# Kernel tuning notes

Hardware: AMD Instinct MI355X
Metric: run time of the kernel (lower is better)

## Reference

```python
import jax, jax.numpy as jnp
import numpy as np

DIM, K_RANK, L, N_CLASS = 64, 16, 8, 10
H = 1e-3
B = 256
DD = DIM * DIM  # 4096


def _cay(C, D):
    # Cayley transform of B = C @ D^T : I + C (I - 0.5 D^T C)^{-1} D^T
    Id = jnp.eye(C.shape[1], dtype=C.dtype)
    DT = jnp.swapaxes(D, 1, 2)
    inv = jnp.linalg.inv(Id - 0.5 * DT @ C)
    return Id + C @ inv @ DT


def setup_inputs() -> dict:
    key = jax.random.key(0)
    ks = jax.random.split(key, 9)
    u = jax.random.normal(ks[0], (B, DIM, K_RANK), jnp.float32) / np.float32(np.sqrt(DIM))
    vh = jax.random.normal(ks[1], (B, K_RANK, DIM), jnp.float32) / np.float32(np.sqrt(DIM))
    eye_k = jnp.eye(K_RANK, dtype=jnp.float32)
    off = 0.05 * jax.random.normal(ks[2], (B, K_RANK, K_RANK), jnp.float32) * (1.0 - eye_k)
    dvals = jax.random.uniform(ks[3], (B, K_RANK), jnp.float32, 0.5, 1.5)
    s_core = off + dvals[:, :, None] * eye_k  # diag bounded away from 0 (invert_S)
    s_block = jnp.zeros((B, DIM, K_RANK), jnp.float32).at[:, :K_RANK, :K_RANK].set(s_core)
    X = jnp.stack([u.reshape(B, -1), s_block.reshape(B, -1), vh.reshape(B, -1)], axis=1)
    sc = np.float32(1.0 / np.sqrt(DD))
    W0 = sc * jax.random.normal(ks[4], (DD, DD), jnp.float32)
    W = sc * jax.random.normal(ks[5], (L, DD, DD), jnp.float32)
    b = sc * jax.random.normal(ks[6], (L, DD), jnp.float32)
    Wc = sc * jax.random.normal(ks[7], (N_CLASS, DD), jnp.float32)
    bc = sc * jax.random.normal(ks[8], (N_CLASS,), jnp.float32)
    return {"X": X, "W0": W0, "W": W, "b": b, "Wc": Wc, "bc": bc}


def reference(X, W0, W, b, Wc, bc):
    Bn = X.shape[0]
    u = X[:, 0].reshape(Bn, DIM, K_RANK)
    s = X[:, 1].reshape(Bn, DIM, K_RANK)[:, :K_RANK, :K_RANK]
    vh = X[:, 2].reshape(Bn, K_RANK, DIM)
    v = jnp.swapaxes(vh, 1, 2)
    eye_k = jnp.eye(K_RANK, dtype=X.dtype)
    eye_d = jnp.eye(DIM, dtype=X.dtype)
    Xf = (u @ s @ vh).reshape(Bn, DD)
    outs = []
    for i in range(L + 1):  # layer 0 has no bias
        lin = Xf @ W0.T if i == 0 else Xf @ W[i - 1].T + b[i - 1]
        dY = jax.nn.relu(lin).reshape(Bn, DIM, DIM)
        # invert_S: invert only the diagonal of s
        s_inv = (1.0 / jnp.diagonal(s, axis1=1, axis2=2))[:, :, None] * eye_k
        dU = dY @ v @ s_inv
        dV = jnp.swapaxes(dY, 1, 2) @ u @ jnp.swapaxes(s_inv, 1, 2)
        dS = jnp.swapaxes(u, 1, 2) @ dY @ v
        uT = jnp.swapaxes(u, 1, 2)
        F = (eye_d - u @ uT) @ dU
        FT = jnp.swapaxes(F, 1, 2)
        u = _cay(H * (F @ uT), -H * (u @ FT)) @ u
        vT = jnp.swapaxes(v, 1, 2)
        F = (eye_d - v @ vT) @ dV
        FT = jnp.swapaxes(F, 1, 2)
        v = _cay(H * (F @ vT), -H * (v @ FT)) @ v
        s = s + H * dS
        Xf = (u @ s @ jnp.swapaxes(v, 1, 2)).reshape(Bn, DD)
        outs.append(Xf)
    X_transformed = jnp.stack(outs, axis=-1)  # (B, dim*dim, L+1)
    X_classified = Xf @ Wc.T + bc
    X_predicted = jax.nn.softmax(X_classified, axis=1)
    return X_predicted, X_classified, X_transformed
```

## Files before the change

### kernel.cpp

```cpp
#include <hip/hip_runtime.h>
#include <math.h>

typedef unsigned short u16;
typedef unsigned int u32;
using bf16x8 = __attribute__((ext_vector_type(8))) short;
using f32x4  = __attribute__((ext_vector_type(4))) float;

#define DD 4096
#define NB 256
#define SPLIT_K 4
#define PSTRIDE (NB * DD)
#define PLANE (NB * DD)

__device__ __forceinline__ u16 f2bf(float f) {
  unsigned int u = __float_as_uint(f);
  u += 0x7fffu + ((u >> 16) & 1u);
  return (u16)(u >> 16);
}
__device__ __forceinline__ float bf2f(u16 h) {
  return __uint_as_float((u32)h << 16);
}
__device__ __forceinline__ unsigned int pack2bf(float a, float b) {
  return (unsigned int)f2bf(a) | ((unsigned int)f2bf(b) << 16);
}
__device__ __forceinline__ void async_cp16(const u16* g, u16* l) {
  __builtin_amdgcn_global_load_lds(
      (const __attribute__((address_space(1))) unsigned int*)g,
      (__attribute__((address_space(3))) unsigned int*)l, 16, 0, 0);
}

__global__ __launch_bounds__(512) void gemm_kernel(
    const u16* __restrict__ A, const float* __restrict__ W,
    u16* __restrict__ part)
{
  const int nt = blockIdx.x;
  const int kz = blockIdx.y;
  const int t = threadIdx.x;
  const int w = t >> 6, l = t & 63;

  __shared__ __align__(16) u16 As[3][256 * 64];
  __shared__ __align__(16) u16 Bs[2][64 * 64];

  const int colg0 = nt << 6;
  const int k0 = kz << 10;

  f32x4 acc[4][2];
#pragma unroll
  for (int mi = 0; mi < 4; ++mi)
#pragma unroll
    for (int nj = 0; nj < 2; ++nj)
      acc[mi][nj] = (f32x4){0.f, 0.f, 0.f, 0.f};

  const int wm = w & 3, wn = w >> 2;
  const int lr = l & 15, lg = l >> 4;
  const int arow_l = (w << 3) + (l >> 3);
  const int acl = l & 7;
  const int bn_l = t >> 3;
  const int bcc = t & 7;

  float4 bs0[3], bs1[3];

#define ISSUE_A(tt, buf) do {                                                \
    const int kkk = k0 + ((tt) << 6);                                        \
    _Pragma("unroll")                                                        \
    for (int r = 0; r < 4; ++r) {                                            \
      const int row = (r << 6) + arow_l;                                     \
      const int cs = acl ^ (row & 7);                                        \
      async_cp16(A + ((size_t)row << 12) + kkk + (cs << 3),                  \
                 &As[buf][(r << 12) + (w << 9)]);                            \
    } } while (0)

#define LOAD_B(tt, set) do {                                                 \
    const float* wsrc = W + ((size_t)(colg0 + bn_l) << 12) + k0 +            \
                        ((tt) << 6) + (bcc << 3);                            \
    bs0[set] = *reinterpret_cast<const float4*>(wsrc);                       \
    bs1[set] = *reinterpret_cast<const float4*>(wsrc + 4);                   \
  } while (0)

  ISSUE_A(0, 0); LOAD_B(0, 0);
  ISSUE_A(1, 1); LOAD_B(1, 1);

#pragma unroll
  for (int tt = 0; tt < 16; ++tt) {
    const int cb = tt % 3, nb = (tt + 2) % 3, pb = tt & 1;
    if (tt + 2 < 16) { ISSUE_A(tt + 2, nb); LOAD_B(tt + 2, nb); }
    if (tt < 14)       { asm volatile("s_waitcnt vmcnt(12)" ::: "memory"); }
    else if (tt == 14) { asm volatile("s_waitcnt vmcnt(6)"  ::: "memory"); }
    else               { asm volatile("s_waitcnt vmcnt(0)"  ::: "memory"); }
    __builtin_amdgcn_sched_barrier(0);
    {
      uint4 pk;
      pk.x = pack2bf(bs0[cb].x, bs0[cb].y);
      pk.y = pack2bf(bs0[cb].z, bs0[cb].w);
      pk.z = pack2bf(bs1[cb].x, bs1[cb].y);
      pk.w = pack2bf(bs1[cb].z, bs1[cb].w);
      *reinterpret_cast<uint4*>(&Bs[pb][(bn_l << 6) + ((bcc ^ (bn_l & 7)) << 3)]) = pk;
    }
    asm volatile("s_waitcnt lgkmcnt(0)" ::: "memory");
    __builtin_amdgcn_s_barrier();
    __builtin_amdgcn_sched_barrier(0);
#pragma unroll
    for (int ks = 0; ks < 2; ++ks) {
      const int cg = (ks << 2) + lg;
      bf16x8 av[4], bv[2];
#pragma unroll
      for (int mi = 0; mi < 4; ++mi) {
        const int fr = (wm << 6) + (mi << 4) + lr;
        av[mi] = *reinterpret_cast<const bf16x8*>(&As[cb][(fr << 6) + ((cg ^ (fr & 7)) << 3)]);
      }
#pragma unroll
      for (int nj = 0; nj < 2; ++nj) {
        const int fc = (wn << 5) + (nj << 4) + lr;
        bv[nj] = *reinterpret_cast<const bf16x8*>(&Bs[pb][(fc << 6) + ((cg ^ (fc & 7)) << 3)]);
      }
#pragma unroll
      for (int mi = 0; mi < 4; ++mi)
#pragma unroll
        for (int nj = 0; nj < 2; ++nj)
          acc[mi][nj] = __builtin_amdgcn_mfma_f32_16x16x32_bf16(
              av[mi], bv[nj], acc[mi][nj], 0, 0, 0);
    }
    __builtin_amdgcn_s_barrier();
  }
#undef ISSUE_A
#undef LOAD_B

  u16* pout = part + (size_t)kz * PSTRIDE;
#pragma unroll
  for (int mi = 0; mi < 4; ++mi)
#pragma unroll
    for (int nj = 0; nj < 2; ++nj) {
      const int col = colg0 + (wn << 5) + (nj << 4) + lr;
#pragma unroll
      for (int j = 0; j < 4; ++j) {
        const int row = (wm << 6) + (mi << 4) + (lg << 2) + j;
        pout[((size_t)row << 12) + col] = f2bf(acc[mi][nj][j]);
      }
    }
}

__device__ __forceinline__ void stiefel_update512(
    float (&Am)[64][17], float (&Dm)[64][17], float (&Fm)[64][17],
    float (&T1)[16][17], float (&G1)[16][17], float (&G2)[16][17],
    float (&M1)[16][17], float (&RS)[512],
    int t, float* __restrict__ gout, size_t ub)
{
  const int p = t >> 3;
  const int j0 = (t << 1) & 15;
  {
    const int half = t & 1, i = t >> 5, j = (t >> 1) & 15;
    float a = 0.f;
    const int r0 = half << 5;
    for (int r = r0; r < r0 + 32; ++r) a += Am[r][i] * Dm[r][j];
    RS[t] = a;
  }
  __syncthreads();
  if (t < 256) T1[t >> 4][t & 15] = RS[t << 1] + RS[(t << 1) + 1];
  __syncthreads();
  {
    float f0 = Dm[p][j0], f1 = Dm[p][j0 + 1];
    for (int k = 0; k < 16; ++k) {
      const float ak = Am[p][k];
      f0 -= ak * T1[k][j0];
      f1 -= ak * T1[k][j0 + 1];
    }
    Fm[p][j0] = f0; Fm[p][j0 + 1] = f1;
  }
  __syncthreads();
  if (t < 256) {
    const int i = t >> 4, j = t & 15;
    float g = 0.f;
    for (int r = 0; r < 64; ++r) g += Am[r][i] * Fm[r][j];
    G1[i][j] = g;
  } else {
    const int tt = t - 256, i = tt >> 4, j = tt & 15;
    float g = 0.f;
    for (int r = 0; r < 64; ++r) g += Am[r][i] * Am[r][j];
    G2[i][j] = g;
  }
  __syncthreads();
  if (t < 256) {
    const int i = t >> 4, j = t & 15;
    float m = 0.f;
    for (int k = 0; k < 16; ++k) m += G1[i][k] * G2[k][j];
    M1[i][j] = m;
  }
  __syncthreads();
  {
    float a0 = 0.f, a1 = 0.f;
    for (int k = 0; k < 16; ++k) {
      const float fk = Fm[p][k];
      a0 += fk * M1[k][j0];
      a1 += fk * M1[k][j0 + 1];
    }
    const float n0 = Am[p][j0] - 1e-6f * a0;
    const float n1 = Am[p][j0 + 1] - 1e-6f * a1;
    __syncthreads();
    Am[p][j0] = n0; Am[p][j0 + 1] = n1;
    *reinterpret_cast<float2*>(gout + ub + (p << 4) + j0) = make_float2(n0, n1);
  }
  __syncthreads();
}

__global__ __launch_bounds__(512) void update_kernel(
    const u16* __restrict__ part, const float* __restrict__ bias,
    float* __restrict__ u_g, float* __restrict__ v_g, float* __restrict__ s_g,
    float* __restrict__ Xf, u16* __restrict__ Xfb,
    float* __restrict__ outL, int layer)
{
  const int b = blockIdx.x, t = threadIdx.x;
  __shared__ float dY[64][68];
  __shared__ float U[64][17], V[64][17];
  __shared__ float P[64][17], Q[64][17], F[64][17];
  __shared__ float S[16][16], dSs[16][17], T1[16][17], G1[16][17], G2[16][17], M1[16][17];
  __shared__ float sinv[16];
  __shared__ float RS[512];

  const size_t ub = (size_t)b << 10;
  {
    const float2 u2 = *reinterpret_cast<const float2*>(u_g + ub + (t << 1));
    const float2 v2 = *reinterpret_cast<const float2*>(v_g + ub + (t << 1));
    const int r = t >> 3, c = (t & 7) << 1;
    U[r][c] = u2.x; U[r][c + 1] = u2.y;
    V[r][c] = v2.x; V[r][c + 1] = v2.y;
    if (t < 256) S[t >> 4][t & 15] = s_g[((size_t)b << 8) + t];
  }
  __syncthreads();
  if (t < 16) sinv[t] = 1.0f / S[t][t];
  {
    const u16* p0 = part + ((size_t)b << 12) + (t << 3);
    float x[8];
#pragma unroll
    for (int e = 0; e < 8; ++e) x[e] = 0.f;
#pragma unroll
    for (int kzi = 0; kzi < 4; ++kzi) {
      const uint4 v = *reinterpret_cast<const uint4*>(p0 + (size_t)kzi * PSTRIDE);
      x[0] += bf2f((u16)(v.x & 0xffff)); x[1] += bf2f((u16)(v.x >> 16));
      x[2] += bf2f((u16)(v.y & 0xffff)); x[3] += bf2f((u16)(v.y >> 16));
      x[4] += bf2f((u16)(v.z & 0xffff)); x[5] += bf2f((u16)(v.z >> 16));
      x[6] += bf2f((u16)(v.w & 0xffff)); x[7] += bf2f((u16)(v.w >> 16));
    }
    if (bias != nullptr) {
      const float4 b0 = *reinterpret_cast<const float4*>(bias + (t << 3));
      const float4 b1 = *reinterpret_cast<const float4*>(bias + (t << 3) + 4);
      x[0] += b0.x; x[1] += b0.y; x[2] += b0.z; x[3] += b0.w;
      x[4] += b1.x; x[5] += b1.y; x[6] += b1.z; x[7] += b1.w;
    }
    const int r = t >> 3, c = (t & 7) << 3;
    float4* d0 = reinterpret_cast<float4*>(&dY[r][c]);
    d0[0] = make_float4(fmaxf(x[0], 0.f), fmaxf(x[1], 0.f), fmaxf(x[2], 0.f), fmaxf(x[3], 0.f));
    d0[1] = make_float4(fmaxf(x[4], 0.f), fmaxf(x[5], 0.f), fmaxf(x[6], 0.f), fmaxf(x[7], 0.f));
  }
  __syncthreads();
  const int p = t >> 3;
  const int j0 = (t << 1) & 15;
  {
    float a0 = 0.f, a1 = 0.f;
    for (int q = 0; q < 64; ++q) {
      const float d = dY[p][q];
      a0 += d * V[q][j0];
      a1 += d * V[q][j0 + 1];
    }
    P[p][j0] = a0; P[p][j0 + 1] = a1;
    float b0 = 0.f, b1 = 0.f;
    for (int r = 0; r < 64; ++r) {
      const float d = dY[r][p];
      b0 += d * U[r][j0];
      b1 += d * U[r][j0 + 1];
    }
    Q[p][j0] = b0; Q[p][j0 + 1] = b1;
  }
  __syncthreads();
  {
    const int half = t & 1, i = t >> 5, j = (t >> 1) & 15;
    float a = 0.f;
    const int r0 = half << 5;
    for (int r = r0; r < r0 + 32; ++r) a += U[r][i] * P[r][j];
    RS[t] = a;
  }
  __syncthreads();
  if (t < 256) dSs[t >> 4][t & 15] = RS[t << 1] + RS[(t << 1) + 1];
  __syncthreads();
  for (int i = t; i < 1024; i += 512) {
    const int r = i >> 4, c = i & 15;
    const float sc = sinv[c];
    P[r][c] *= sc;
    Q[r][c] *= sc;
  }
  __syncthreads();

  stiefel_update512(U, P, F, T1, G1, G2, M1, RS, t, u_g, ub);
  stiefel_update512(V, Q, F, T1, G1, G2, M1, RS, t, v_g, ub);

  if (t < 256) {
    const int i = t >> 4, j = t & 15;
    const float ns = S[i][j] + 1e-3f * dSs[i][j];
    S[i][j] = ns;
    s_g[((size_t)b << 8) + t] = ns;
  }
  __syncthreads();
  {
    float a0 = 0.f, a1 = 0.f;
    for (int k = 0; k < 16; ++k) {
      const float uk = U[p][k];
      a0 += uk * S[k][j0];
      a1 += uk * S[k][j0 + 1];
    }
    P[p][j0] = a0; P[p][j0 + 1] = a1;
  }
  __syncthreads();
  {
    const int q0 = (t & 7) << 3;
    float res[8];
#pragma unroll
    for (int e = 0; e < 8; ++e) res[e] = 0.f;
    for (int i = 0; i < 16; ++i) {
      const float pi = P[p][i];
#pragma unroll
      for (int e = 0; e < 8; ++e) res[e] += pi * V[q0 + e][i];
    }
    const size_t ko = ((size_t)b << 12) + (p << 6) + q0;
    float4* xo = reinterpret_cast<float4*>(Xf + ko);
    xo[0] = make_float4(res[0], res[1], res[2], res[3]);
    xo[1] = make_float4(res[4], res[5], res[6], res[7]);
    uint4 pk;
    pk.x = pack2bf(res[0], res[1]); pk.y = pack2bf(res[2], res[3]);
    pk.z = pack2bf(res[4], res[5]); pk.w = pack2bf(res[6], res[7]);
    *reinterpret_cast<uint4*>(Xfb + ko) = pk;
    float4* op = reinterpret_cast<float4*>(outL + (size_t)layer * PLANE + ko);
    op[0] = xo[0]; op[1] = xo[1];
  }
}

__global__ __launch_bounds__(256) void pack_kernel(
    const float* __restrict__ outL, float* __restrict__ outT)
{
  const int t = threadIdx.x;
  const int base = blockIdx.x << 8;
  __shared__ float buf[256 * 9];
#pragma unroll
  for (int l = 0; l < 9; ++l)
    buf[t * 9 + l] = outL[(size_t)l * PLANE + base + t];
  __syncthreads();
  const float4* b4 = reinterpret_cast<const float4*>(buf);
  float4* o4 = reinterpret_cast<float4*>(outT + (size_t)base * 9);
  for (int i = t; i < 576; i += 256) o4[i] = b4[i];
}

__global__ __launch_bounds__(256) void init_kernel(
    const float* __restrict__ X, float* __restrict__ u_g, float* __restrict__ v_g,
    float* __restrict__ s_g, float* __restrict__ Xf, u16* __restrict__ Xfb)
{
  const int b = blockIdx.x, t = threadIdx.x;
  __shared__ float U[64][17], V[64][17], S[16][16], P[64][17];
  const float* xb = X + (size_t)b * 3072;
  const size_t ub = (size_t)b << 10;
  {
    const float4 u4 = *reinterpret_cast<const float4*>(xb + (t << 2));
    const int r = t >> 2, c = (t & 3) << 2;
    U[r][c] = u4.x; U[r][c + 1] = u4.y; U[r][c + 2] = u4.z; U[r][c + 3] = u4.w;
    *reinterpret_cast<float4*>(u_g + ub + (t << 2)) = u4;
    const float sv = xb[1024 + t];
    S[t >> 4][t & 15] = sv;
    s_g[((size_t)b << 8) + t] = sv;
    const float4 v4 = *reinterpret_cast<const float4*>(xb + 2048 + (t << 2));
    const int g = t << 2;
    const int iv = g >> 6, q = g & 63;
    V[q][iv] = v4.x; V[q + 1][iv] = v4.y; V[q + 2][iv] = v4.z; V[q + 3][iv] = v4.w;
    v_g[ub + (size_t)q * 16 + iv] = v4.x;
    v_g[ub + (size_t)(q + 1) * 16 + iv] = v4.y;
    v_g[ub + (size_t)(q + 2) * 16 + iv] = v4.z;
    v_g[ub + (size_t)(q + 3) * 16 + iv] = v4.w;
  }
  __syncthreads();
  const int p4 = t >> 2, e4 = (t & 3) << 2;
#pragma unroll
  for (int e = 0; e < 4; ++e) {
    float a = 0.f;
    for (int i = 0; i < 16; ++i) a += U[p4][i] * S[i][e4 + e];
    P[p4][e4 + e] = a;
  }
  __syncthreads();
  {
    const int q0 = (t & 3) << 4;
    float res[16];
#pragma unroll
    for (int qq = 0; qq < 16; ++qq) {
      float a = 0.f;
      for (int i = 0; i < 16; ++i) a += P[p4][i] * V[q0 + qq][i];
      res[qq] = a;
    }
    const size_t ko = ((size_t)b << 12) + (p4 << 6) + q0;
    float4* xo = reinterpret_cast<float4*>(Xf + ko);
    xo[0] = make_float4(res[0], res[1], res[2], res[3]);
    xo[1] = make_float4(res[4], res[5], res[6], res[7]);
    xo[2] = make_float4(res[8], res[9], res[10], res[11]);
    xo[3] = make_float4(res[12], res[13], res[14], res[15]);
    uint4 pk0, pk1;
    pk0.x = pack2bf(res[0], res[1]);   pk0.y = pack2bf(res[2], res[3]);
    pk0.z = pack2bf(res[4], res[5]);   pk0.w = pack2bf(res[6], res[7]);
    pk1.x = pack2bf(res[8], res[9]);   pk1.y = pack2bf(res[10], res[11]);
    pk1.z = pack2bf(res[12], res[13]); pk1.w = pack2bf(res[14], res[15]);
    *reinterpret_cast<uint4*>(Xfb + ko) = pk0;
    *reinterpret_cast<uint4*>(Xfb + ko + 8) = pk1;
  }
}

__global__ __launch_bounds__(256) void classifier_kernel(
    const float* __restrict__ Xf, const float* __restrict__ Wc,
    const float* __restrict__ bc, float* __restrict__ pred, float* __restrict__ cls)
{
  const int b = blockIdx.x, t = threadIdx.x;
  const int lane = t & 63, w = t >> 6;
  __shared__ float red[4][10];
  float acc[10];
#pragma unroll
  for (int c = 0; c < 10; ++c) acc[c] = 0.f;
  const float* xr = Xf + ((size_t)b << 12);
  for (int k = t; k < 4096; k += 256) {
    const float x = xr[k];
#pragma unroll
    for (int c = 0; c < 10; ++c) acc[c] += x * Wc[c * 4096 + k];
  }
#pragma unroll
  for (int c = 0; c < 10; ++c)
    for (int off = 32; off; off >>= 1) acc[c] += __shfl_xor(acc[c], off);
  if (lane == 0)
#pragma unroll
    for (int c = 0; c < 10; ++c) red[w][c] = acc[c];
  __syncthreads();
  if (t == 0) {
    float lg[10], ex[10];
    float m = -1e30f;
#pragma unroll
    for (int c = 0; c < 10; ++c) {
      lg[c] = red[0][c] + red[1][c] + red[2][c] + red[3][c] + bc[c];
      m = fmaxf(m, lg[c]);
    }
    float s = 0.f;
#pragma unroll
    for (int c = 0; c < 10; ++c) { ex[c] = expf(lg[c] - m); s += ex[c]; }
    const float inv = 1.f / s;
#pragma unroll
    for (int c = 0; c < 10; ++c) {
      cls[b * 10 + c] = lg[c];
      pred[b * 10 + c] = ex[c] * inv;
    }
  }
}

extern "C" void kernel_launch(void* const* d_in, const int* in_sizes, int n_in,
                              void* d_out, int out_size, void* d_ws, size_t ws_size,
                              hipStream_t stream) {
  (void)in_sizes; (void)n_in; (void)out_size; (void)ws_size;
  const float* X  = (const float*)d_in[0];
  const float* W0 = (const float*)d_in[1];
  const float* W  = (const float*)d_in[2];
  const float* bb = (const float*)d_in[3];
  const float* Wc = (const float*)d_in[4];
  const float* bc = (const float*)d_in[5];

  float* out_pred  = (float*)d_out;
  float* out_cls   = out_pred + 2560;
  float* out_trans = out_pred + 5120;

  char* ws = (char*)d_ws;
  float* Xf   = (float*)(ws);
  u16*   part = (u16*)  (ws + (4ull << 20));
  float* u_g  = (float*)(ws + (20ull << 20));
  float* v_g  = (float*)(ws + (21ull << 20));
  float* s_g  = (float*)(ws + (22ull << 20));
  u16*   Xfb  = (u16*)  (ws + (23ull << 20));
  float* outL = (float*)(ws + (25ull << 20));

  init_kernel<<<NB, 256, 0, stream>>>(X, u_g, v_g, s_g, Xf, Xfb);
  for (int i = 0; i <= 8; ++i) {
    const float* Wl = (i == 0) ? W0 : W + (size_t)(i - 1) * DD * DD;
    gemm_kernel<<<dim3(64, SPLIT_K), 512, 0, stream>>>(Xfb, Wl, part);
    update_kernel<<<NB, 512, 0, stream>>>(
        part, (i == 0) ? nullptr : (bb + (size_t)(i - 1) * DD),
        u_g, v_g, s_g, Xf, Xfb, outL, i);
  }
  pack_kernel<<<4096, 256, 0, stream>>>(outL, out_trans);
  classifier_kernel<<<NB, 256, 0, stream>>>(Xf, Wc, bc, out_pred, out_cls);
}
```

Before: 487.1 us.

## Fuse all layer kernels into one cooperative persistent kernel with grid syncs

Replaces the init, per-layer gemm and update, pack and classifier launches with a single cooperative kernel of 256 blocks. Grid-wide syncs separate the phases, and shared memory is aliased across phases through a union of structs. The aim is to remove about 20 kernel launches and their inter-kernel gaps. The cost is grid.sync overhead, and the GEMM now runs with launch_bounds(512,2), which may constrain registers and occupancy.

```diff
diff --git a/kernel.cpp b/kernel.cpp
--- a/kernel.cpp
+++ b/kernel.cpp
@@ -1,5 +1,8 @@
 #include <hip/hip_runtime.h>
+#include <hip/hip_cooperative_groups.h>
 #include <math.h>
+
+namespace cg = cooperative_groups;
 
 typedef unsigned short u16;
 typedef unsigned int u32;
@@ -29,18 +32,26 @@
       (__attribute__((address_space(3))) unsigned int*)l, 16, 0, 0);
 }
 
-__global__ __launch_bounds__(512) void gemm_kernel(
-    const u16* __restrict__ A, const float* __restrict__ W,
-    u16* __restrict__ part)
-{
-  const int nt = blockIdx.x;
-  const int kz = blockIdx.y;
-  const int t = threadIdx.x;
+struct GemmSmem {
+  u16 As[3][256 * 64];
+  u16 Bs[2][64 * 64];
+};
+struct UpdSmem {
+  float dY[64][68];
+  float U[64][17], V[64][17], P[64][17], Q[64][17], F[64][17];
+  float S[16][16], dSs[16][17], T1[16][17], G1[16][17], G2[16][17], M1[16][17];
+  float sinv[16];
+  float RS[512];
+};
+struct PackSmem { float buf[512 * 9]; };
+struct ClsSmem  { float red[8][10]; };
+
+__device__ __forceinline__ void gemm_phase(
+    GemmSmem& sm, const u16* __restrict__ A, const float* __restrict__ W,
+    u16* __restrict__ part, int g, int t)
+{
+  const int nt = g & 63, kz = g >> 6;
   const int w = t >> 6, l = t & 63;
-
-  __shared__ __align__(16) u16 As[3][256 * 64];
-  __shared__ __align__(16) u16 Bs[2][64 * 64];
-
   const int colg0 = nt << 6;
   const int k0 = kz << 10;
 
@@ -67,7 +78,7 @@
       const int row = (r << 6) + arow_l;                                     \
       const int cs = acl ^ (row & 7);                                        \
       async_cp16(A + ((size_t)row << 12) + kkk + (cs << 3),                  \
-                 &As[buf][(r << 12) + (w << 9)]);                            \
+                 &sm.As[buf][(r << 12) + (w << 9)]);                         \
     } } while (0)
 
 #define LOAD_B(tt, set) do {                                                 \
@@ -94,24 +105,24 @@
       pk.y = pack2bf(bs0[cb].z, bs0[cb].w);
       pk.z = pack2bf(bs1[cb].x, bs1[cb].y);
       pk.w = pack2bf(bs1[cb].z, bs1[cb].w);
-      *reinterpret_cast<uint4*>(&Bs[pb][(bn_l << 6) + ((bcc ^ (bn_l & 7)) << 3)]) = pk;
+      *reinterpret_cast<uint4*>(&sm.Bs[pb][(bn_l << 6) + ((bcc ^ (bn_l & 7)) << 3)]) = pk;
     }
     asm volatile("s_waitcnt lgkmcnt(0)" ::: "memory");
     __builtin_amdgcn_s_barrier();
     __builtin_amdgcn_sched_barrier(0);
 #pragma unroll
     for (int ks = 0; ks < 2; ++ks) {
-      const int cg = (ks << 2) + lg;
+      const int cg2 = (ks << 2) + lg;
       bf16x8 av[4], bv[2];
 #pragma unroll
       for (int mi = 0; mi < 4; ++mi) {
         const int fr = (wm << 6) + (mi << 4) + lr;
-        av[mi] = *reinterpret_cast<const bf16x8*>(&As[cb][(fr << 6) + ((cg ^ (fr & 7)) << 3)]);
+        av[mi] = *reinterpret_cast<const bf16x8*>(&sm.As[cb][(fr << 6) + ((cg2 ^ (fr & 7)) << 3)]);
       }
 #pragma unroll
       for (int nj = 0; nj < 2; ++nj) {
         const int fc = (wn << 5) + (nj << 4) + lr;
-        bv[nj] = *reinterpret_cast<const bf16x8*>(&Bs[pb][(fc << 6) + ((cg ^ (fc & 7)) << 3)]);
+        bv[nj] = *reinterpret_cast<const bf16x8*>(&sm.Bs[pb][(fc << 6) + ((cg2 ^ (fc & 7)) << 3)]);
       }
 #pragma unroll
       for (int mi = 0; mi < 4; ++mi)
@@ -140,9 +151,7 @@
 }
 
 __device__ __forceinline__ void stiefel_update512(
-    float (&Am)[64][17], float (&Dm)[64][17], float (&Fm)[64][17],
-    float (&T1)[16][17], float (&G1)[16][17], float (&G2)[16][17],
-    float (&M1)[16][17], float (&RS)[512],
+    UpdSmem& m, float (&Am)[64][17], float (&Dm)[64][17],
     int t, float* __restrict__ gout, size_t ub)
 {
   const int p = t >> 3;
@@ -152,46 +161,46 @@
     float a = 0.f;
     const int r0 = half << 5;
     for (int r = r0; r < r0 + 32; ++r) a += Am[r][i] * Dm[r][j];
-    RS[t] = a;
-  }
-  __syncthreads();
-  if (t < 256) T1[t >> 4][t & 15] = RS[t << 1] + RS[(t << 1) + 1];
+    m.RS[t] = a;
+  }
+  __syncthreads();
+  if (t < 256) m.T1[t >> 4][t & 15] = m.RS[t << 1] + m.RS[(t << 1) + 1];
   __syncthreads();
   {
     float f0 = Dm[p][j0], f1 = Dm[p][j0 + 1];
     for (int k = 0; k < 16; ++k) {
       const float ak = Am[p][k];
-      f0 -= ak * T1[k][j0];
-      f1 -= ak * T1[k][j0 + 1];
-    }
-    Fm[p][j0] = f0; Fm[p][j0 + 1] = f1;
+      f0 -= ak * m.T1[k][j0];
+      f1 -= ak * m.T1[k][j0 + 1];
+    }
+    m.F[p][j0] = f0; m.F[p][j0 + 1] = f1;
   }
   __syncthreads();
   if (t < 256) {
     const int i = t >> 4, j = t & 15;
     float g = 0.f;
-    for (int r = 0; r < 64; ++r) g += Am[r][i] * Fm[r][j];
-    G1[i][j] = g;
+    for (int r = 0; r < 64; ++r) g += Am[r][i] * m.F[r][j];
+    m.G1[i][j] = g;
   } else {
     const int tt = t - 256, i = tt >> 4, j = tt & 15;
     float g = 0.f;
     for (int r = 0; r < 64; ++r) g += Am[r][i] * Am[r][j];
-    G2[i][j] = g;
+    m.G2[i][j] = g;
   }
   __syncthreads();
   if (t < 256) {
     const int i = t >> 4, j = t & 15;
-    float m = 0.f;
-    for (int k = 0; k < 16; ++k) m += G1[i][k] * G2[k][j];
-    M1[i][j] = m;
+    float mm = 0.f;
+    for (int k = 0; k < 16; ++k) mm += m.G1[i][k] * m.G2[k][j];
+    m.M1[i][j] = mm;
   }
   __syncthreads();
   {
     float a0 = 0.f, a1 = 0.f;
     for (int k = 0; k < 16; ++k) {
-      const float fk = Fm[p][k];
-      a0 += fk * M1[k][j0];
-      a1 += fk * M1[k][j0 + 1];
+      const float fk = m.F[p][k];
+      a0 += fk * m.M1[k][j0];
+      a1 += fk * m.M1[k][j0 + 1];
     }
     const float n0 = Am[p][j0] - 1e-6f * a0;
     const float n1 = Am[p][j0 + 1] - 1e-6f * a1;
@@ -202,31 +211,65 @@
   __syncthreads();
 }
 
-__global__ __launch_bounds__(512) void update_kernel(
-    const u16* __restrict__ part, const float* __restrict__ bias,
+__device__ __forceinline__ void write_xf_tail(
+    UpdSmem& m, int t, int b, float* __restrict__ Xf, u16* __restrict__ Xfb,
+    float* __restrict__ outL_plane)
+{
+  const int p = t >> 3;
+  const int j0 = (t << 1) & 15;
+  {
+    float a0 = 0.f, a1 = 0.f;
+    for (int k = 0; k < 16; ++k) {
+      const float uk = m.U[p][k];
+      a0 += uk * m.S[k][j0];
+      a1 += uk * m.S[k][j0 + 1];
+    }
+    m.P[p][j0] = a0; m.P[p][j0 + 1] = a1;
+  }
+  __syncthreads();
+  {
+    const int q0 = (t & 7) << 3;
+    float res[8];
+#pragma unroll
+    for (int e = 0; e < 8; ++e) res[e] = 0.f;
+    for (int i = 0; i < 16; ++i) {
+      const float pi = m.P[p][i];
+#pragma unroll
+      for (int e = 0; e < 8; ++e) res[e] += pi * m.V[q0 + e][i];
+    }
+    const size_t ko = ((size_t)b << 12) + (p << 6) + q0;
+    float4* xo = reinterpret_cast<float4*>(Xf + ko);
+    const float4 r0 = make_float4(res[0], res[1], res[2], res[3]);
+    const float4 r1 = make_float4(res[4], res[5], res[6], res[7]);
+    xo[0] = r0; xo[1] = r1;
+    uint4 pk;
+    pk.x = pack2bf(res[0], res[1]); pk.y = pack2bf(res[2], res[3]);
+    pk.z = pack2bf(res[4], res[5]); pk.w = pack2bf(res[6], res[7]);
+    *reinterpret_cast<uint4*>(Xfb + ko) = pk;
+    if (outL_plane != nullptr) {
+      float4* op = reinterpret_cast<float4*>(outL_plane + ko);
+      op[0] = r0; op[1] = r1;
+    }
+  }
+}
+
+__device__ __forceinline__ void update_phase(
+    UpdSmem& m, const u16* __restrict__ part, const float* __restrict__ bias,
     float* __restrict__ u_g, float* __restrict__ v_g, float* __restrict__ s_g,
     float* __restrict__ Xf, u16* __restrict__ Xfb,
-    float* __restrict__ outL, int layer)
-{
-  const int b = blockIdx.x, t = threadIdx.x;
-  __shared__ float dY[64][68];
-  __shared__ float U[64][17], V[64][17];
-  __shared__ float P[64][17], Q[64][17], F[64][17];
-  __shared__ float S[16][16], dSs[16][17], T1[16][17], G1[16][17], G2[16][17], M1[16][17];
-  __shared__ float sinv[16];
-  __shared__ float RS[512];
-
+    float* __restrict__ outL_plane, int b, int t)
+{
   const size_t ub = (size_t)b << 10;
   {
     const float2 u2 = *reinterpret_cast<const float2*>(u_g + ub + (t << 1));
     const float2 v2 = *reinterpret_cast<const float2*>(v_g + ub + (t << 1));
     const int r = t >> 3, c = (t & 7) << 1;
-    U[r][c] = u2.x; U[r][c + 1] = u2.y;
-    V[r][c] = v2.x; V[r][c + 1] = v2.y;
-    if (t < 256) S[t >> 4][t & 15] = s_g[((size_t)b << 8) + t];
-  }
-  __syncthreads();
-  if (t < 16) sinv[t] = 1.0f / S[t][t];
+    m.U[r][c] = u2.x; m.U[r][c + 1] = u2.y;
+    m.V[r][c] = v2.x; m.V[r][c + 1] = v2.y;
+    if (t < 256) m.S[t >> 4][t & 15] = s_g[((size_t)b << 8) + t];
+  }
+  __syncthreads();
+  if (t < 16) m.sinv[t] = 1.0f / m.S[t][t];
   {
     const u16* p0 = part + ((size_t)b << 12) + (t << 3);
     float x[8];
@@ -247,7 +290,7 @@
       x[4] += b1.x; x[5] += b1.y; x[6] += b1.z; x[7] += b1.w;
     }
     const int r = t >> 3, c = (t & 7) << 3;
-    float4* d0 = reinterpret_cast<float4*>(&dY[r][c]);
+    float4* d0 = reinterpret_cast<float4*>(&m.dY[r][c]);
     d0[0] = make_float4(fmaxf(x[0], 0.f), fmaxf(x[1], 0.f), fmaxf(x[2], 0.f), fmaxf(x[3], 0.f));
     d0[1] = make_float4(fmaxf(x[4], 0.f), fmaxf(x[5], 0.f), fmaxf(x[6], 0.f), fmaxf(x[7], 0.f));
   }
@@ -257,195 +300,162 @@
   {
     float a0 = 0.f, a1 = 0.f;
     for (int q = 0; q < 64; ++q) {
-      const float d = dY[p][q];
-      a0 += d * V[q][j0];
-      a1 += d * V[q][j0 + 1];
-    }
-    P[p][j0] = a0; P[p][j0 + 1] = a1;
+      const float d = m.dY[p][q];
+      a0 += d * m.V[q][j0];
+      a1 += d * m.V[q][j0 + 1];
+    }
+    m.P[p][j0] = a0; m.P[p][j0 + 1] = a1;
     float b0 = 0.f, b1 = 0.f;
     for (int r = 0; r < 64; ++r) {
-      const float d = dY[r][p];
-      b0 += d * U[r][j0];
-      b1 += d * U[r][j0 + 1];
-    }
-    Q[p][j0] = b0; Q[p][j0 + 1] = b1;
+      const float d = m.dY[r][p];
+      b0 += d * m.U[r][j0];
+      b1 += d * m.U[r][j0 + 1];
+    }
+    m.Q[p][j0] = b0; m.Q[p][j0 + 1] = b1;
   }
   __syncthreads();
   {
     const int half = t & 1, i = t >> 5, j = (t >> 1) & 15;
     float a = 0.f;
     const int r0 = half << 5;
-    for (int r = r0; r < r0 + 32; ++r) a += U[r][i] * P[r][j];
-    RS[t] = a;
-  }
-  __syncthreads();
-  if (t < 256) dSs[t >> 4][t & 15] = RS[t << 1] + RS[(t << 1) + 1];
+    for (int r = r0; r < r0 + 32; ++r) a += m.U[r][i] * m.P[r][j];
+    m.RS[t] = a;
+  }
+  __syncthreads();
+  if (t < 256) m.dSs[t >> 4][t & 15] = m.RS[t << 1] + m.RS[(t << 1) + 1];
   __syncthreads();
   for (int i = t; i < 1024; i += 512) {
     const int r = i >> 4, c = i & 15;
-    const float sc = sinv[c];
-    P[r][c] *= sc;
-    Q[r][c] *= sc;
-  }
-  __syncthreads();
-
-  stiefel_update512(U, P, F, T1, G1, G2, M1, RS, t, u_g, ub);
-  stiefel_update512(V, Q, F, T1, G1, G2, M1, RS, t, v_g, ub);
+    const float sc = m.sinv[c];
+    m.P[r][c] *= sc;
+    m.Q[r][c] *= sc;
+  }
+  __syncthreads();
+
+  stiefel_update512(m, m.U, m.P, t, u_g, ub);
+  stiefel_update512(m, m.V, m.Q, t, v_g, ub);
 
   if (t < 256) {
     const int i = t >> 4, j = t & 15;
-    const float ns = S[i][j] + 1e-3f * dSs[i][j];
-    S[i][j] = ns;
+    const float ns = m.S[i][j] + 1e-3f * m.dSs[i][j];
+    m.S[i][j] = ns;
     s_g[((size_t)b << 8) + t] = ns;
   }
   __syncthreads();
-  {
-    float a0 = 0.f, a1 = 0.f;
-    for (int k = 0; k < 16; ++k) {
-      const float uk = U[p][k];
-      a0 += uk * S[k][j0];
-      a1 += uk * S[k][j0 + 1];
-    }
-    P[p][j0] = a0; P[p][j0 + 1] = a1;
-  }
-  __syncthreads();
-  {
-    const int q0 = (t & 7) << 3;
-    float res[8];
-#pragma unroll
-    for (int e = 0; e < 8; ++e) res[e] = 0.f;
-    for (int i = 0; i < 16; ++i) {
-      const float pi = P[p][i];
-#pragma unroll
-      for (int e = 0; e < 8; ++e) res[e] += pi * V[q0 + e][i];
-    }
-    const size_t ko = ((size_t)b << 12) + (p << 6) + q0;
-    float4* xo = reinterpret_cast<float4*>(Xf + ko);
-    xo[0] = make_float4(res[0], res[1], res[2], res[3]);
-    xo[1] = make_float4(res[4], res[5], res[6], res[7]);
-    uint4 pk;
-    pk.x = pack2bf(res[0], res[1]); pk.y = pack2bf(res[2], res[3]);
-    pk.z = pack2bf(res[4], res[5]); pk.w = pack2bf(res[6], res[7]);
-    *reinterpret_cast<uint4*>(Xfb + ko) = pk;
-    float4* op = reinterpret_cast<float4*>(outL + (size_t)layer * PLANE + ko);
-    op[0] = xo[0]; op[1] = xo[1];
-  }
-}
-
-__global__ __launch_bounds__(256) void pack_kernel(
-    const float* __restrict__ outL, float* __restrict__ outT)
-{
-  const int t = threadIdx.x;
-  const int base = blockIdx.x << 8;
-  __shared__ float buf[256 * 9];
-#pragma unroll
-  for (int l = 0; l < 9; ++l)
-    buf[t * 9 + l] = outL[(size_t)l * PLANE + base + t];
-  __syncthreads();
-  const float4* b4 = reinterpret_cast<const float4*>(buf);
-  float4* o4 = reinterpret_cast<float4*>(outT + (size_t)base * 9);
-  for (int i = t; i < 576; i += 256) o4[i] = b4[i];
-}
-
-__global__ __launch_bounds__(256) void init_kernel(
-    const float* __restrict__ X, float* __restrict__ u_g, float* __restrict__ v_g,
-    float* __restrict__ s_g, float* __restrict__ Xf, u16* __restrict__ Xfb)
-{
-  const int b = blockIdx.x, t = threadIdx.x;
-  __shared__ float U[64][17], V[64][17], S[16][16], P[64][17];
+  write_xf_tail(m, t, b, Xf, Xfb, outL_plane);
+}
+
+__device__ __forceinline__ void init_phase(
+    UpdSmem& m, const float* __restrict__ X,
+    float* __restrict__ u_g, float* __restrict__ v_g, float* __restrict__ s_g,
+    float* __restrict__ Xf, u16* __restrict__ Xfb, int b, int t)
+{
   const float* xb = X + (size_t)b * 3072;
   const size_t ub = (size_t)b << 10;
   {
-    const float4 u4 = *reinterpret_cast<const float4*>(xb + (t << 2));
-    const int r = t >> 2, c = (t & 3) << 2;
-    U[r][c] = u4.x; U[r][c + 1] = u4.y; U[r][c + 2] = u4.z; U[r][c + 3] = u4.w;
-    *reinterpret_cast<float4*>(u_g + ub + (t << 2)) = u4;
-    const float sv = xb[1024 + t];
-    S[t >> 4][t & 15] = sv;
-    s_g[((size_t)b << 8) + t] = sv;
-    const float4 v4 = *reinterpret_cast<const float4*>(xb + 2048 + (t << 2));
-    const int g = t << 2;
-    const int iv = g >> 6, q = g & 63;
-    V[q][iv] = v4.x; V[q + 1][iv] = v4.y; V[q + 2][iv] = v4.z; V[q + 3][iv] = v4.w;
-    v_g[ub + (size_t)q * 16 + iv] = v4.x;
-    v_g[ub + (size_t)(q + 1) * 16 + iv] = v4.y;
-    v_g[ub + (size_t)(q + 2) * 16 + iv] = v4.z;
-    v_g[ub + (size_t)(q + 3) * 16 + iv] = v4.w;
-  }
-  __syncthreads();
-  const int p4 = t >> 2, e4 = (t & 3) << 2;
-#pragma unroll
-  for (int e = 0; e < 4; ++e) {
-    float a = 0.f;
-    for (int i = 0; i < 16; ++i) a += U[p4][i] * S[i][e4 + e];
-    P[p4][e4 + e] = a;
-  }
-  __syncthreads();
-  {
-    const int q0 = (t & 3) << 4;
-    float res[16];
-#pragma unroll
-    for (int qq = 0; qq < 16; ++qq) {
-      float a = 0.f;
-      for (int i = 0; i < 16; ++i) a += P[p4][i] * V[q0 + qq][i];
-      res[qq] = a;
-    }
-    const size_t ko = ((size_t)b << 12) + (p4 << 6) + q0;
-    float4* xo = reinterpret_cast<float4*>(Xf + ko);
-    xo[0] = make_float4(res[0], res[1], res[2], res[3]);
-    xo[1] = make_float4(res[4], res[5], res[6], res[7]);
-    xo[2] = make_float4(res[8], res[9], res[10], res[11]);
-    xo[3] = make_float4(res[12], res[13], res[14], res[15]);
-    uint4 pk0, pk1;
-    pk0.x = pack2bf(res[0], res[1]);   pk0.y = pack2bf(res[2], res[3]);
-    pk0.z = pack2bf(res[4], res[5]);   pk0.w = pack2bf(res[6], res[7]);
-    pk1.x = pack2bf(res[8], res[9]);   pk1.y = pack2bf(res[10], res[11]);
-    pk1.z = pack2bf(res[12], res[13]); pk1.w = pack2bf(res[14], res[15]);
-    *reinterpret_cast<uint4*>(Xfb + ko) = pk0;
-    *reinterpret_cast<uint4*>(Xfb + ko + 8) = pk1;
-  }
-}
-
-__global__ __launch_bounds__(256) void classifier_kernel(
-    const float* __restrict__ Xf, const float* __restrict__ Wc,
-    const float* __restrict__ bc, float* __restrict__ pred, float* __restrict__ cls)
-{
-  const int b = blockIdx.x, t = threadIdx.x;
-  const int lane = t & 63, w = t >> 6;
-  __shared__ float red[4][10];
-  float acc[10];
-#pragma unroll
-  for (int c = 0; c < 10; ++c) acc[c] = 0.f;
-  const float* xr = Xf + ((size_t)b << 12);
-  for (int k = t; k < 4096; k += 256) {
-    const float x = xr[k];
-#pragma unroll
-    for (int c = 0; c < 10; ++c) acc[c] += x * Wc[c * 4096 + k];
-  }
-#pragma unroll
-  for (int c = 0; c < 10; ++c)
-    for (int off = 32; off; off >>= 1) acc[c] += __shfl_xor(acc[c], off);
-  if (lane == 0)
-#pragma unroll
-    for (int c = 0; c < 10; ++c) red[w][c] = acc[c];
-  __syncthreads();
-  if (t == 0) {
-    float lg[10], ex[10];
-    float m = -1e30f;
-#pragma unroll
-    for (int c = 0; c < 10; ++c) {
-      lg[c] = red[0][c] + red[1][c] + red[2][c] + red[3][c] + bc[c];
-      m = fmaxf(m, lg[c]);
-    }
-    float s = 0.f;
-#pragma unroll
-    for (int c = 0; c < 10; ++c) { ex[c] = expf(lg[c] - m); s += ex[c]; }
-    const float inv = 1.f / s;
-#pragma unroll
-    for (int c = 0; c < 10; ++c) {
-      cls[b * 10 + c] = lg[c];
-      pred[b * 10 + c] = ex[c] * inv;
-    }
+    const float2 u2 = *reinterpret_cast<const float2*>(xb + (t << 1));
+    const int r = t >> 3, c = (t & 7) << 1;
+    m.U[r][c] = u2.x; m.U[r][c + 1] = u2.y;
+    *reinterpret_cast<float2*>(u_g + ub + (t << 1)) = u2;
+    if (t < 256) {
+      const float sv = xb[1024 + t];
+      m.S[t >> 4][t & 15] = sv;
+      s_g[((size_t)b << 8) + t] = sv;
+    }
+    const float2 v2 = *reinterpret_cast<const float2*>(xb + 2048 + (t << 1));
+    const int g2 = t << 1;
+    const int iv = g2 >> 6, q = g2 & 63;
+    m.V[q][iv] = v2.x; m.V[q + 1][iv] = v2.y;
+    v_g[ub + (size_t)q * 16 + iv] = v2.x;
+    v_g[ub + (size_t)(q + 1) * 16 + iv] = v2.y;
+  }
+  __syncthreads();
+  write_xf_tail(m, t, b, Xf, Xfb, nullptr);
+}
+
+__global__ __launch_bounds__(512, 2) void mega_kernel(
+    const float* __restrict__ X, const float* __restrict__ W0,
+    const float* __restrict__ W, const float* __restrict__ bb,
+    const float* __restrict__ Wc, const float* __restrict__ bc,
+    float* __restrict__ pred, float* __restrict__ cls, float* __restrict__ outT,
+    float* __restrict__ Xf, u16* __restrict__ part,
+    float* __restrict__ u_g, float* __restrict__ v_g, float* __restrict__ s_g,
+    u16* __restrict__ Xfb, float* __restrict__ outL)
+{
+  cg::grid_group grid = cg::this_grid();
+  __shared__ __align__(16) char smem_raw[sizeof(GemmSmem)];
+  GemmSmem& gs = *reinterpret_cast<GemmSmem*>(smem_raw);
+  UpdSmem&  us = *reinterpret_cast<UpdSmem*>(smem_raw);
+  PackSmem& ps = *reinterpret_cast<PackSmem*>(smem_raw);
+  ClsSmem&  cs = *reinterpret_cast<ClsSmem*>(smem_raw);
+
+  const int g = blockIdx.x, t = threadIdx.x;
+
+  init_phase(us, X, u_g, v_g, s_g, Xf, Xfb, g, t);
+  grid.sync();
+
+  for (int layer = 0; layer <= 8; ++layer) {
+    const float* Wl = (layer == 0) ? W0 : W + (size_t)(layer - 1) * DD * DD;
+    gemm_phase(gs, Xfb, Wl, part, g, t);
+    grid.sync();
+    update_phase(us, part, (layer == 0) ? nullptr : (bb + (size_t)(layer - 1) * DD),
+                 u_g, v_g, s_g, Xf, Xfb,
+                 outL + (size_t)layer * PLANE, g, t);
+    grid.sync();
+  }
+
+  {
+    const int lane = t & 63, w = t >> 6;
+    float acc[10];
+#pragma unroll
+    for (int c = 0; c < 10; ++c) acc[c] = 0.f;
+    const float* xr = Xf + ((size_t)g << 12);
+    for (int k = t; k < 4096; k += 512) {
+      const float x = xr[k];
+#pragma unroll
+      for (int c = 0; c < 10; ++c) acc[c] += x * Wc[c * 4096 + k];
+    }
+#pragma unroll
+    for (int c = 0; c < 10; ++c)
+      for (int off = 32; off; off >>= 1) acc[c] += __shfl_xor(acc[c], off);
+    if (lane == 0)
+#pragma unroll
+      for (int c = 0; c < 10; ++c) cs.red[w][c] = acc[c];
+    __syncthreads();
+    if (t == 0) {
+      float lg[10], ex[10];
+      float mx = -1e30f;
+#pragma unroll
+      for (int c = 0; c < 10; ++c) {
+        float s8 = 0.f;
+#pragma unroll
+        for (int ww = 0; ww < 8; ++ww) s8 += cs.red[ww][c];
+        lg[c] = s8 + bc[c];
+        mx = fmaxf(mx, lg[c]);
+      }
+      float s = 0.f;
+#pragma unroll
+      for (int c = 0; c < 10; ++c) { ex[c] = expf(lg[c] - mx); s += ex[c]; }
+      const float inv = 1.f / s;
+#pragma unroll
+      for (int c = 0; c < 10; ++c) {
+        cls[g * 10 + c] = lg[c];
+        pred[g * 10 + c] = ex[c] * inv;
+      }
+    }
+    __syncthreads();
+  }
+
+  for (int it = 0; it < 8; ++it) {
+    const int base = ((g << 3) + it) << 9;
+#pragma unroll
+    for (int l = 0; l < 9; ++l)
+      ps.buf[t * 9 + l] = outL[(size_t)l * PLANE + base + t];
+    __syncthreads();
+    const float4* b4 = reinterpret_cast<const float4*>(ps.buf);
+    float4* o4 = reinterpret_cast<float4*>(outT + (size_t)base * 9);
+    for (int i = t; i < 1152; i += 512) o4[i] = b4[i];
+    __syncthreads();
   }
 }
 
@@ -473,14 +483,12 @@
   u16*   Xfb  = (u16*)  (ws + (23ull << 20));
   float* outL = (float*)(ws + (25ull << 20));
 
-  init_kernel<<<NB, 256, 0, stream>>>(X, u_g, v_g, s_g, Xf, Xfb);
-  for (int i = 0; i <= 8; ++i) {
-    const float* Wl = (i == 0) ? W0 : W + (size_t)(i - 1) * DD * DD;
-    gemm_kernel<<<dim3(64, SPLIT_K), 512, 0, stream>>>(Xfb, Wl, part);
-    update_kernel<<<NB, 512, 0, stream>>>(
-        part, (i == 0) ? nullptr : (bb + (size_t)(i - 1) * DD),
-        u_g, v_g, s_g, Xf, Xfb, outL, i);
-  }
-  pack_kernel<<<4096, 256, 0, stream>>>(outL, out_trans);
-  classifier_kernel<<<NB, 256, 0, stream>>>(Xf, Wc, bc, out_pred, out_cls);
-}
+  void* kargs[] = {
+    (void*)&X, (void*)&W0, (void*)&W, (void*)&bb, (void*)&Wc, (void*)&bc,
+    (void*)&out_pred, (void*)&out_cls, (void*)&out_trans,
+    (void*)&Xf, (void*)&part, (void*)&u_g, (void*)&v_g, (void*)&s_g,
+    (void*)&Xfb, (void*)&outL
+  };
+  hipLaunchCooperativeKernel((const void*)mega_kernel, dim3(256), dim3(512),
+                             kargs, 0, stream);
+}
```

Result: slower. 1.186 ms (+143.5%).

## Double split-K, drop GEMM software pipeline for single-buffer LDS with higher occupancy

Applied to the files above, without the earlier changes.

Changes the split-K factor from 4 to 8, so each GEMM block covers 512 K elements and the grid has twice as many blocks. The triple-buffered async A / double-buffered B pipeline is replaced by single buffers with plain __syncthreads. A launch-bounds hint asks for 4 blocks per CU. The intent is to gain latency hiding from occupancy rather than in-block prefetch, while the reduction in the epilogue kernel now reads 8 partial planes. The Xf store reuse is also tidied to avoid reading back from global memory. This costs double the partial-sum write and read traffic and exposes load latency within each block. The part buffer (allocation not shown) must also be large enough for 8 planes.

```diff
diff --git a/kernel.cpp b/kernel.cpp
--- a/kernel.cpp
+++ b/kernel.cpp
@@ -8,7 +8,7 @@
 
 #define DD 4096
 #define NB 256
-#define SPLIT_K 4
+#define SPLIT_K 8
 #define PSTRIDE (NB * DD)
 #define PLANE (NB * DD)
 
@@ -29,7 +29,7 @@
       (__attribute__((address_space(3))) unsigned int*)l, 16, 0, 0);
 }
 
-__global__ __launch_bounds__(512) void gemm_kernel(
+__global__ __launch_bounds__(512, 4) void gemm_kernel(
     const u16* __restrict__ A, const float* __restrict__ W,
     u16* __restrict__ part)
 {
@@ -38,11 +38,11 @@
   const int t = threadIdx.x;
   const int w = t >> 6, l = t & 63;
 
-  __shared__ __align__(16) u16 As[3][256 * 64];
-  __shared__ __align__(16) u16 Bs[2][64 * 64];
+  __shared__ __align__(16) u16 As[256 * 64];
+  __shared__ __align__(16) u16 Bs[64 * 64];
 
   const int colg0 = nt << 6;
-  const int k0 = kz << 10;
+  const int k0 = kz << 9;
 
   f32x4 acc[4][2];
 #pragma unroll
@@ -58,47 +58,28 @@
   const int bn_l = t >> 3;
   const int bcc = t & 7;
 
-  float4 bs0[3], bs1[3];
-
-#define ISSUE_A(tt, buf) do {                                                \
-    const int kkk = k0 + ((tt) << 6);                                        \
-    _Pragma("unroll")                                                        \
-    for (int r = 0; r < 4; ++r) {                                            \
-      const int row = (r << 6) + arow_l;                                     \
-      const int cs = acl ^ (row & 7);                                        \
-      async_cp16(A + ((size_t)row << 12) + kkk + (cs << 3),                  \
-                 &As[buf][(r << 12) + (w << 9)]);                            \
-    } } while (0)
-
-#define LOAD_B(tt, set) do {                                                 \
-    const float* wsrc = W + ((size_t)(colg0 + bn_l) << 12) + k0 +            \
-                        ((tt) << 6) + (bcc << 3);                            \
-    bs0[set] = *reinterpret_cast<const float4*>(wsrc);                       \
-    bs1[set] = *reinterpret_cast<const float4*>(wsrc + 4);                   \
-  } while (0)
-
-  ISSUE_A(0, 0); LOAD_B(0, 0);
-  ISSUE_A(1, 1); LOAD_B(1, 1);
-
-#pragma unroll
-  for (int tt = 0; tt < 16; ++tt) {
-    const int cb = tt % 3, nb = (tt + 2) % 3, pb = tt & 1;
-    if (tt + 2 < 16) { ISSUE_A(tt + 2, nb); LOAD_B(tt + 2, nb); }
-    if (tt < 14)       { asm volatile("s_waitcnt vmcnt(12)" ::: "memory"); }
-    else if (tt == 14) { asm volatile("s_waitcnt vmcnt(6)"  ::: "memory"); }
-    else               { asm volatile("s_waitcnt vmcnt(0)"  ::: "memory"); }
-    __builtin_amdgcn_sched_barrier(0);
+  for (int tt = 0; tt < 8; ++tt) {
+    const int kk = k0 + (tt << 6);
+    __syncthreads();
+#pragma unroll
+    for (int r = 0; r < 4; ++r) {
+      const int row = (r << 6) + arow_l;
+      const int cs = acl ^ (row & 7);
+      async_cp16(A + ((size_t)row << 12) + kk + (cs << 3),
+                 &As[(r << 12) + (w << 9)]);
+    }
     {
+      const float* wsrc = W + ((size_t)(colg0 + bn_l) << 12) + kk + (bcc << 3);
+      const float4 f0 = *reinterpret_cast<const float4*>(wsrc);
+      const float4 f1 = *reinterpret_cast<const float4*>(wsrc + 4);
       uint4 pk;
-      pk.x = pack2bf(bs0[cb].x, bs0[cb].y);
-      pk.y = pack2bf(bs0[cb].z, bs0[cb].w);
-      pk.z = pack2bf(bs1[cb].x, bs1[cb].y);
-      pk.w = pack2bf(bs1[cb].z, bs1[cb].w);
-      *reinterpret_cast<uint4*>(&Bs[pb][(bn_l << 6) + ((bcc ^ (bn_l & 7)) << 3)]) = pk;
-    }
-    asm volatile("s_waitcnt lgkmcnt(0)" ::: "memory");
-    __builtin_amdgcn_s_barrier();
-    __builtin_amdgcn_sched_barrier(0);
+      pk.x = pack2bf(f0.x, f0.y);
+      pk.y = pack2bf(f0.z, f0.w);
+      pk.z = pack2bf(f1.x, f1.y);
+      pk.w = pack2bf(f1.z, f1.w);
+      *reinterpret_cast<uint4*>(&Bs[(bn_l << 6) + ((bcc ^ (bn_l & 7)) << 3)]) = pk;
+    }
+    __syncthreads();
 #pragma unroll
     for (int ks = 0; ks < 2; ++ks) {
       const int cg = (ks << 2) + lg;
@@ -106,12 +87,12 @@
 #pragma unroll
       for (int mi = 0; mi < 4; ++mi) {
         const int fr = (wm << 6) + (mi << 4) + lr;
-        av[mi] = *reinterpret_cast<const bf16x8*>(&As[cb][(fr << 6) + ((cg ^ (fr & 7)) << 3)]);
+        av[mi] = *reinterpret_cast<const bf16x8*>(&As[(fr << 6) + ((cg ^ (fr & 7)) << 3)]);
       }
 #pragma unroll
       for (int nj = 0; nj < 2; ++nj) {
         const int fc = (wn << 5) + (nj << 4) + lr;
-        bv[nj] = *reinterpret_cast<const bf16x8*>(&Bs[pb][(fc << 6) + ((cg ^ (fc & 7)) << 3)]);
+        bv[nj] = *reinterpret_cast<const bf16x8*>(&Bs[(fc << 6) + ((cg ^ (fc & 7)) << 3)]);
       }
 #pragma unroll
       for (int mi = 0; mi < 4; ++mi)
@@ -120,10 +101,7 @@
           acc[mi][nj] = __builtin_amdgcn_mfma_f32_16x16x32_bf16(
               av[mi], bv[nj], acc[mi][nj], 0, 0, 0);
     }
-    __builtin_amdgcn_s_barrier();
-  }
-#undef ISSUE_A
-#undef LOAD_B
+  }
 
   u16* pout = part + (size_t)kz * PSTRIDE;
 #pragma unroll
@@ -233,7 +211,7 @@
 #pragma unroll
     for (int e = 0; e < 8; ++e) x[e] = 0.f;
 #pragma unroll
-    for (int kzi = 0; kzi < 4; ++kzi) {
+    for (int kzi = 0; kzi < SPLIT_K; ++kzi) {
       const uint4 v = *reinterpret_cast<const uint4*>(p0 + (size_t)kzi * PSTRIDE);
       x[0] += bf2f((u16)(v.x & 0xffff)); x[1] += bf2f((u16)(v.x >> 16));
       x[2] += bf2f((u16)(v.y & 0xffff)); x[3] += bf2f((u16)(v.y >> 16));
@@ -321,14 +299,15 @@
     }
     const size_t ko = ((size_t)b << 12) + (p << 6) + q0;
     float4* xo = reinterpret_cast<float4*>(Xf + ko);
-    xo[0] = make_float4(res[0], res[1], res[2], res[3]);
-    xo[1] = make_float4(res[4], res[5], res[6], res[7]);
+    const float4 r0 = make_float4(res[0], res[1], res[2], res[3]);
+    const float4 r1 = make_float4(res[4], res[5], res[6], res[7]);
+    xo[0] = r0; xo[1] = r1;
     uint4 pk;
     pk.x = pack2bf(res[0], res[1]); pk.y = pack2bf(res[2], res[3]);
     pk.z = pack2bf(res[4], res[5]); pk.w = pack2bf(res[6], res[7]);
     *reinterpret_cast<uint4*>(Xfb + ko) = pk;
     float4* op = reinterpret_cast<float4*>(outL + (size_t)layer * PLANE + ko);
-    op[0] = xo[0]; op[1] = xo[1];
+    op[0] = r0; op[1] = r1;
   }
 }
 
```

After: 439.1 us. 1.11x faster.
